# Kernel tuning notes

Measured on AMD Instinct MI355X. Metric: run time of the kernel, lower is better.

## Reference

```python
import jax, jax.numpy as jnp
import numpy as np

B, T, D = 16, 4096, 128   # batch, frames (75 Hz), latent dim
N_Q, K = 8, 1024          # RVQ stages (bandwidth 6 kbps), codebook size


def setup_inputs() -> dict:
    key = jax.random.key(0)
    kx, ke = jax.random.split(key)
    x = jax.random.normal(kx, (B, T, D), dtype=jnp.float32)
    # Residual-VQ codebooks, one [K, D] table per stage (scale=1.0 applied).
    embed = jax.random.normal(ke, (N_Q, K, D), dtype=jnp.float32)
    return {"x": x, "embed": embed}


def reference(x, embed):
    """Residual vector quantization: per stage, nearest-codebook lookup and
    residual subtraction. Returns codes with shape [n_q, B, T] (int32),
    matching encodec's stacked per-stage indices (stage-first layout, as the
    original module's `y[-1]` slicing implies)."""

    def step(residual, e):
        # residual: [B, T, D], e: [K, D]
        # argmin ||r - e||^2 == argmax (2 r.e - ||e||^2); ||r||^2 is constant in k.
        dots = jnp.einsum('btd,kd->btk', residual, e)          # [B, T, K]
        dist = 2.0 * dots - jnp.sum(e * e, axis=-1)            # [B, T, K]
        codes = jnp.argmax(dist, axis=-1).astype(jnp.int32)    # [B, T]
        quantized = e[codes]                                   # gather -> [B, T, D]
        return residual - quantized, codes

    _, codes = jax.lax.scan(step, x, embed)  # codes: [N_Q, B, T]
    return codes
```

## Files before the change

kernel.cpp:

```cpp
#include <hip/hip_runtime.h>

#define M_TOTAL 65536
#define DDIM    128
#define KCODES  1024
#define NQ      8
#define RROWS   64
#define NC      64
#define NCHUNKS (KCODES / NC)
#define CHUNK_B (NC * DDIM * 2)
#define BIAS    320.0f
#define THRQ    0.106f

typedef _Float16 half8 __attribute__((ext_vector_type(8)));
typedef float    f32x4 __attribute__((ext_vector_type(4)));
typedef unsigned u32x2 __attribute__((ext_vector_type(2)));

__device__ __forceinline__ unsigned umx(unsigned a, unsigned b) { return a > b ? a : b; }
__device__ __forceinline__ unsigned umn(unsigned a, unsigned b) { return a < b ? a : b; }

__device__ __forceinline__ void gld_lds16(const void* g, void* l) {
  __builtin_amdgcn_global_load_lds(
      (const __attribute__((address_space(1))) unsigned int*)g,
      (__attribute__((address_space(3))) unsigned int*)l, 16, 0, 0);
}

__global__ __launch_bounds__(256) void enorm_kernel(const float* __restrict__ embed,
                                                    float* __restrict__ enorm) {
  int c = blockIdx.x * 4 + (threadIdx.x >> 6);
  int lane = threadIdx.x & 63;
  const float* e = embed + (size_t)c * DDIM;
  float v0 = e[lane];
  float v1 = e[lane + 64];
  float s = fmaf(v0, v0, v1 * v1);
  #pragma unroll
  for (int off = 32; off > 0; off >>= 1) s += __shfl_down(s, off);
  if (lane == 0) enorm[c] = s;
}

__global__ __launch_bounds__(256) void esplit16_kernel(const float* __restrict__ embed,
                                                       _Float16* __restrict__ Ef16) {
  unsigned u = blockIdx.x * 256 + threadIdx.x;
  size_t src = (size_t)u * 8;
  float4 v0 = *(const float4*)(embed + src);
  float4 v1 = *(const float4*)(embed + src + 4);
  half8 h;
  h[0] = (_Float16)v0.x; h[1] = (_Float16)v0.y; h[2] = (_Float16)v0.z; h[3] = (_Float16)v0.w;
  h[4] = (_Float16)v1.x; h[5] = (_Float16)v1.y; h[6] = (_Float16)v1.z; h[7] = (_Float16)v1.w;
  unsigned row = u >> 4;
  unsigned j   = u & 15;
  size_t dst = (size_t)row * 128 + 8 * (j ^ (row & 7));
  *(half8*)(Ef16 + dst) = h;
}

__global__ __launch_bounds__(256, 2) void rvq_fused(
    const float* __restrict__ x,
    const float* __restrict__ embed,
    const _Float16* __restrict__ Ef16,
    const float* __restrict__ enorm,
    int* __restrict__ codes)
{
  __shared__ __attribute__((aligned(16))) float resid[RROWS][132];
  __shared__ __attribute__((aligned(16))) char EsU[2 * CHUNK_B];
  __shared__ unsigned redk[RROWS][2][2];
  __shared__ int bcode[RROWS];
  __shared__ int frows[RROWS];
  __shared__ int fcnt;

  const int tid = threadIdx.x;
  const int wv = tid >> 6;
  const int lane = tid & 63;
  const int l15 = lane & 15;
  const int q = lane >> 4;
  const int rw = wv & 1;
  const int cw = wv >> 1;
  const int row_base = blockIdx.x * RROWS;
  const int rx = cw * 32 + l15;
  const int xr = rx & 7;

  #pragma unroll
  for (int it = 0; it < 8; ++it) {
    int idx = it * 256 + tid;
    int r = idx >> 5, f4 = idx & 31;
    *(float4*)(&resid[r][f4 * 4]) = *(const float4*)(x + (size_t)(row_base + r) * DDIM + f4 * 4);
  }
  if (tid == 0) fcnt = 0;
  __syncthreads();

  for (int st = 0; st < NQ; ++st) {
    const _Float16* EfS = Ef16 + (size_t)st * KCODES * DDIM;
    const float* enS = enorm + (size_t)st * KCODES;
    const float* embS = embed + (size_t)st * KCODES * DDIM;

    half8 af[2][4];
    #pragma unroll
    for (int rt = 0; rt < 2; ++rt) {
      const float* pa = &resid[rw * 32 + rt * 16 + l15][0];
      #pragma unroll
      for (int kc = 0; kc < 4; ++kc) {
        float4 x0 = *(const float4*)(pa + kc * 32 + q * 8);
        float4 x1 = *(const float4*)(pa + kc * 32 + q * 8 + 4);
        half8 h;
        h[0] = (_Float16)x0.x; h[1] = (_Float16)x0.y; h[2] = (_Float16)x0.z; h[3] = (_Float16)x0.w;
        h[4] = (_Float16)x1.x; h[5] = (_Float16)x1.y; h[6] = (_Float16)x1.z; h[7] = (_Float16)x1.w;
        af[rt][kc] = h;
      }
    }

    {
      const char* g = (const char*)EfS;
      #pragma unroll
      for (int it = 0; it < 4; ++it) {
        const int off = it * 4096 + wv * 1024;
        gld_lds16(g + off + lane * 16, EsU + off);
      }
    }
    float enr0 = enS[cw * 32 + l15];
    float enr1 = enS[cw * 32 + 16 + l15];
    __syncthreads();

    unsigned k1[8], k2[8];
    #pragma unroll
    for (int s = 0; s < 8; ++s) { k1[s] = 0u; k2[s] = 0u; }

    for (int cc = 0; cc < NCHUNKS; ++cc) {
      const int cur = cc & 1;
      if (cc + 1 < NCHUNKS) {
        const char* g = (const char*)EfS + (size_t)(cc + 1) * CHUNK_B;
        char* l = EsU + (cur ^ 1) * CHUNK_B;
        #pragma unroll
        for (int it = 0; it < 4; ++it) {
          const int off = it * 4096 + wv * 1024;
          gld_lds16(g + off + lane * 16, l + off);
        }
      }
      float nh0 = BIAS - 0.5f * enr0;
      float nh1 = BIAS - 0.5f * enr1;
      if (cc + 1 < NCHUNKS) {
        enr0 = enS[(cc + 1) * NC + cw * 32 + l15];
        enr1 = enS[(cc + 1) * NC + cw * 32 + 16 + l15];
      }
      f32x4 acc[2][2];
      #pragma unroll
      for (int rt = 0; rt < 2; ++rt) {
        acc[rt][0] = (f32x4){nh0, nh0, nh0, nh0};
        acc[rt][1] = (f32x4){nh1, nh1, nh1, nh1};
      }

      const char* eb = EsU + cur * CHUNK_B;
      #pragma unroll
      for (int kc = 0; kc < 4; ++kc) {
        const int jswz = 16 * ((kc * 4 + q) ^ xr);
        half8 bf0 = *(const half8*)(eb + rx * 256 + jswz);
        half8 bf1 = *(const half8*)(eb + (rx + 16) * 256 + jswz);
        #pragma unroll
        for (int rt = 0; rt < 2; ++rt) {
          acc[rt][0] = __builtin_amdgcn_mfma_f32_16x16x32_f16(af[rt][kc], bf0, acc[rt][0], 0, 0, 0);
          acc[rt][1] = __builtin_amdgcn_mfma_f32_16x16x32_f16(af[rt][kc], bf1, acc[rt][1], 0, 0, 0);
        }
      }

      const unsigned revb = 1023u - (unsigned)(cc * NC + cw * 32 + l15);
      #pragma unroll
      for (int rt = 0; rt < 2; ++rt)
        #pragma unroll
        for (int reg = 0; reg < 4; ++reg) {
          const int s = rt * 4 + reg;
          unsigned kk0 = (__float_as_uint(acc[rt][0][reg]) & 0xFFFFFC00u) | revb;
          k2[s] = umx(umn(kk0, k1[s]), k2[s]);
          k1[s] = umx(k1[s], kk0);
          unsigned kk1 = (__float_as_uint(acc[rt][1][reg]) & 0xFFFFFC00u) | (revb - 16u);
          k2[s] = umx(umn(kk1, k1[s]), k2[s]);
          k1[s] = umx(k1[s], kk1);
        }
      __syncthreads();
    }

    #pragma unroll
    for (int rt = 0; rt < 2; ++rt)
      #pragma unroll
      for (int reg = 0; reg < 4; ++reg) {
        const int row = rw * 32 + rt * 16 + q * 4 + reg;
        u32x2 kv = {k1[rt * 4 + reg], k2[rt * 4 + reg]};
        *(u32x2*)(EsU + row * 256 + (cw * 16 + l15) * 8) = kv;
      }

    #pragma unroll
    for (int s = 0; s < 8; ++s) {
      #pragma unroll
      for (int off = 1; off < 16; off <<= 1) {
        unsigned o1 = __shfl_xor(k1[s], off);
        unsigned o2 = __shfl_xor(k2[s], off);
        unsigned mn = umn(k1[s], o1);
        k1[s] = umx(k1[s], o1);
        k2[s] = umx(mn, umx(k2[s], o2));
      }
    }
    if (l15 == 0) {
      #pragma unroll
      for (int rt = 0; rt < 2; ++rt)
        #pragma unroll
        for (int reg = 0; reg < 4; ++reg) {
          const int row = rw * 32 + rt * 16 + q * 4 + reg;
          redk[row][cw][0] = k1[rt * 4 + reg];
          redk[row][cw][1] = k2[rt * 4 + reg];
        }
    }
    __syncthreads();

    if (tid < RROWS) {
      unsigned a1 = redk[tid][0][0], a2 = redk[tid][0][1];
      unsigned b1 = redk[tid][1][0], b2 = redk[tid][1][1];
      unsigned f1 = umx(a1, b1);
      unsigned f2 = umx(umn(a1, b1), umx(a2, b2));
      bcode[tid] = 1023 - (int)(f1 & 1023u);
      float d1 = __uint_as_float(f1 & 0xFFFFFC00u);
      float d2 = __uint_as_float(f2 & 0xFFFFFC00u);
      if (d1 - d2 <= THRQ) {
        int p = atomicAdd(&fcnt, 1);
        frows[p] = tid;
      }
    }
    __syncthreads();
    const int nf = fcnt;

    for (int f = wv; f < nf; f += 4) {
      const int r = frows[f];
      const unsigned key = *(const unsigned*)(EsU + r * 256 + (lane >> 1) * 8 + (lane & 1) * 4);
      const int c = 1023 - (int)(key & 1023u);
      const float* rv = &resid[r][0];
      const float* ev = embS + (size_t)c * DDIM;
      float a = 0.f;
      #pragma unroll 4
      for (int k4 = 0; k4 < 32; ++k4) {
        float4 rr = *(const float4*)(rv + k4 * 4);
        float4 e4 = *(const float4*)(ev + k4 * 4);
        a = fmaf(rr.x, e4.x, a); a = fmaf(rr.y, e4.y, a);
        a = fmaf(rr.z, e4.z, a); a = fmaf(rr.w, e4.w, a);
      }
      float bv = 2.0f * a - enS[c];
      int bi = c;
      #pragma unroll
      for (int off = 32; off > 0; off >>= 1) {
        float o = __shfl_down(bv, off);
        int oi = __shfl_down(bi, off);
        if (o > bv || (o == bv && oi < bi)) { bv = o; bi = oi; }
      }
      if (lane == 0) bcode[r] = bi;
    }
    __syncthreads();
    if (tid == 0) fcnt = 0;

    if (tid < RROWS) codes[(size_t)st * M_TOTAL + row_base + tid] = bcode[tid];
    if (st < NQ - 1) {
      #pragma unroll
      for (int it = 0; it < 8; ++it) {
        int idx = it * 256 + tid;
        int r = idx >> 5, f4 = idx & 31;
        float4 e = *(const float4*)(embS + (size_t)bcode[r] * DDIM + f4 * 4);
        float4 a = *(const float4*)(&resid[r][f4 * 4]);
        a.x -= e.x; a.y -= e.y; a.z -= e.z; a.w -= e.w;
        *(float4*)(&resid[r][f4 * 4]) = a;
      }
    }
    __syncthreads();
  }
}

#define F_NCHUNK  256
#define F_KC      16
#define F_AS_STRIDE 68
#define F_ES_STRIDE 260

__global__ __launch_bounds__(256, 3) void rvq_stage_kernel(
    const float* __restrict__ rin, float* __restrict__ rout,
    const float* __restrict__ embed, const float* __restrict__ enorm,
    int* __restrict__ codes)
{
  __shared__ float smem[DDIM * F_AS_STRIDE + F_KC * F_ES_STRIDE + F_NCHUNK];
  float* As  = smem;
  float* Es  = smem + DDIM * F_AS_STRIDE;
  float* Ens = Es + F_KC * F_ES_STRIDE;
  float* red_v = Es;
  int*   red_i = (int*)(Es + 64 * 33);
  int*   bcode = (int*)(Es + 2 * 64 * 33);

  const int tid = threadIdx.x;
  const int tx = tid & 31;
  const int ty = tid >> 5;
  const int row_base = blockIdx.x * 64;

  #pragma unroll
  for (int it = 0; it < 8; ++it) {
    int idx = it * 256 + tid;
    int r = idx >> 5, f4 = idx & 31;
    float4 v = *(const float4*)(rin + (size_t)(row_base + r) * DDIM + f4 * 4);
    As[(4 * f4 + 0) * F_AS_STRIDE + r] = v.x;
    As[(4 * f4 + 1) * F_AS_STRIDE + r] = v.y;
    As[(4 * f4 + 2) * F_AS_STRIDE + r] = v.z;
    As[(4 * f4 + 3) * F_AS_STRIDE + r] = v.w;
  }

  float best[8]; int bidx[8];
  #pragma unroll
  for (int i = 0; i < 8; ++i) { best[i] = -3.0e38f; bidx[i] = 0x7fffffff; }

  for (int nc = 0; nc < KCODES / F_NCHUNK; ++nc) {
    float acc[8][8];
    #pragma unroll
    for (int i = 0; i < 8; ++i)
      #pragma unroll
      for (int j = 0; j < 8; ++j) acc[i][j] = 0.0f;

    for (int kc = 0; kc < DDIM / F_KC; ++kc) {
      __syncthreads();
      #pragma unroll
      for (int it = 0; it < 4; ++it) {
        int idx = it * 256 + tid;
        int c = idx >> 2, f4 = idx & 3;
        float4 v = *(const float4*)(embed + (size_t)(nc * F_NCHUNK + c) * DDIM + kc * F_KC + f4 * 4);
        Es[(4 * f4 + 0) * F_ES_STRIDE + c] = v.x;
        Es[(4 * f4 + 1) * F_ES_STRIDE + c] = v.y;
        Es[(4 * f4 + 2) * F_ES_STRIDE + c] = v.z;
        Es[(4 * f4 + 3) * F_ES_STRIDE + c] = v.w;
      }
      if (kc == 0) Ens[tid] = enorm[nc * F_NCHUNK + tid];
      __syncthreads();

      const float* pa = As + kc * F_KC * F_AS_STRIDE + ty * 8;
      const float* pe = Es + 4 * tx;
      #pragma unroll 4
      for (int k = 0; k < F_KC; ++k) {
        float4 a0 = *(const float4*)(pa + k * F_AS_STRIDE);
        float4 a1 = *(const float4*)(pa + k * F_AS_STRIDE + 4);
        float4 e0 = *(const float4*)(pe + k * F_ES_STRIDE);
        float4 e1 = *(const float4*)(pe + k * F_ES_STRIDE + 128);
        float aa[8] = {a0.x, a0.y, a0.z, a0.w, a1.x, a1.y, a1.z, a1.w};
        float ee[8] = {e0.x, e0.y, e0.z, e0.w, e1.x, e1.y, e1.z, e1.w};
        #pragma unroll
        for (int i = 0; i < 8; ++i)
          #pragma unroll
          for (int j = 0; j < 8; ++j)
            acc[i][j] = fmaf(aa[i], ee[j], acc[i][j]);
      }
    }

    #pragma unroll
    for (int j = 0; j < 8; ++j) {
      int c_local = (j < 4) ? (4 * tx + j) : (128 + 4 * tx + (j - 4));
      float en = Ens[c_local];
      int cg = nc * F_NCHUNK + c_local;
      #pragma unroll
      for (int i = 0; i < 8; ++i) {
        float dist = 2.0f * acc[i][j] - en;
        if (dist > best[i] || (dist == best[i] && cg < bidx[i])) { best[i] = dist; bidx[i] = cg; }
      }
    }
  }

  __syncthreads();
  #pragma unroll
  for (int i = 0; i < 8; ++i) {
    red_v[(ty * 8 + i) * 33 + tx] = best[i];
    red_i[(ty * 8 + i) * 33 + tx] = bidx[i];
  }
  __syncthreads();
  if (tid < 64) {
    float bv = red_v[tid * 33]; int bi = red_i[tid * 33];
    #pragma unroll
    for (int t = 1; t < 32; ++t) {
      float v = red_v[tid * 33 + t]; int ix = red_i[tid * 33 + t];
      if (v > bv || (v == bv && ix < bi)) { bv = v; bi = ix; }
    }
    codes[row_base + tid] = bi;
    bcode[tid] = bi;
  }
  __syncthreads();
  #pragma unroll
  for (int it = 0; it < 32; ++it) {
    int idx = it * 256 + tid;
    int r = idx >> 7, d = idx & 127;
    float e = embed[(size_t)bcode[r] * DDIM + d];
    rout[(size_t)(row_base + r) * DDIM + d] = As[d * F_AS_STRIDE + r] - e;
  }
}

extern "C" void kernel_launch(void* const* d_in, const int* in_sizes, int n_in,
                              void* d_out, int out_size, void* d_ws, size_t ws_size,
                              hipStream_t stream) {
  (void)in_sizes; (void)n_in; (void)out_size;
  const float* x = (const float*)d_in[0];
  const float* embed = (const float*)d_in[1];
  int* codes = (int*)d_out;

  const size_t E16_BYTES = (size_t)NQ * KCODES * DDIM * 2;
  const size_t EN_BYTES  = (size_t)NQ * KCODES * 4;
  const size_t need = E16_BYTES + EN_BYTES + 256;

  if (ws_size >= need) {
    char* w = (char*)d_ws;
    _Float16* Ef16 = (_Float16*)w;     w += E16_BYTES;
    float* enorm   = (float*)w;

    enorm_kernel<<<dim3(NQ * KCODES / 4), dim3(256), 0, stream>>>(embed, enorm);
    esplit16_kernel<<<dim3(NQ * KCODES * DDIM / 8 / 256), dim3(256), 0, stream>>>(embed, Ef16);
    rvq_fused<<<dim3(M_TOTAL / RROWS), dim3(256), 0, stream>>>(
        x, embed, Ef16, enorm, codes);
  } else {
    const size_t resid_elems = (size_t)M_TOTAL * DDIM;
    const bool ws_ok = ws_size >= (resid_elems + (size_t)NQ * KCODES) * sizeof(float);
    float* resid = ws_ok ? (float*)d_ws : (float*)d_in[0];
    float* enorm = ws_ok ? ((float*)d_ws + resid_elems) : (float*)d_ws;

    enorm_kernel<<<dim3(NQ * KCODES / 4), dim3(256), 0, stream>>>(embed, enorm);
    for (int q = 0; q < NQ; ++q) {
      const float* rin = (q == 0) ? x : resid;
      rvq_stage_kernel<<<dim3(M_TOTAL / 64), dim3(256), 0, stream>>>(
          rin, resid, embed + (size_t)q * KCODES * DDIM,
          enorm + (size_t)q * KCODES, codes + (size_t)q * M_TOTAL);
    }
  }
}
```

Baseline: 360.8 us.

## Double fused RVQ block to 512 threads, splitting codes across four wave columns

Raises the fused RVQ kernel from 256 to 512 threads per block, with eight waves where each wave handles 16 codes per chunk instead of 32. Each wave keeps fewer accumulators, and the cross-wave top-2 reduction grows from two to four partial candidates. The fallback recheck now evaluates two candidates per lane. The intent is more waves in flight to hide LDS and MFMA latency, at the cost of per-wave work halving and more barrier and reduction overhead. The launch bound of 4 blocks of 512 threads may also constrain registers.

```diff
diff --git a/kernel.cpp b/kernel.cpp
--- a/kernel.cpp
+++ b/kernel.cpp
@@ -5,6 +5,7 @@
 #define KCODES  1024
 #define NQ      8
 #define RROWS   64
+#define NTHR    512
 #define NC      64
 #define NCHUNKS (KCODES / NC)
 #define CHUNK_B (NC * DDIM * 2)
@@ -52,7 +53,7 @@
   *(half8*)(Ef16 + dst) = h;
 }
 
-__global__ __launch_bounds__(256, 2) void rvq_fused(
+__global__ __launch_bounds__(NTHR, 4) void rvq_fused(
     const float* __restrict__ x,
     const float* __restrict__ embed,
     const _Float16* __restrict__ Ef16,
@@ -61,7 +62,7 @@
 {
   __shared__ __attribute__((aligned(16))) float resid[RROWS][132];
   __shared__ __attribute__((aligned(16))) char EsU[2 * CHUNK_B];
-  __shared__ unsigned redk[RROWS][2][2];
+  __shared__ unsigned redk[RROWS][4][2];
   __shared__ int bcode[RROWS];
   __shared__ int frows[RROWS];
   __shared__ int fcnt;
@@ -74,12 +75,12 @@
   const int rw = wv & 1;
   const int cw = wv >> 1;
   const int row_base = blockIdx.x * RROWS;
-  const int rx = cw * 32 + l15;
+  const int rx = cw * 16 + l15;
   const int xr = rx & 7;
 
   #pragma unroll
-  for (int it = 0; it < 8; ++it) {
-    int idx = it * 256 + tid;
+  for (int it = 0; it < 4; ++it) {
+    int idx = it * NTHR + tid;
     int r = idx >> 5, f4 = idx & 31;
     *(float4*)(&resid[r][f4 * 4]) = *(const float4*)(x + (size_t)(row_base + r) * DDIM + f4 * 4);
   }
@@ -109,13 +110,12 @@
     {
       const char* g = (const char*)EfS;
       #pragma unroll
-      for (int it = 0; it < 4; ++it) {
-        const int off = it * 4096 + wv * 1024;
+      for (int it = 0; it < 2; ++it) {
+        const int off = wv * 2048 + it * 1024;
         gld_lds16(g + off + lane * 16, EsU + off);
       }
     }
-    float enr0 = enS[cw * 32 + l15];
-    float enr1 = enS[cw * 32 + 16 + l15];
+    float enr = enS[cw * 16 + l15];
     __syncthreads();
 
     unsigned k1[8], k2[8];
@@ -128,50 +128,35 @@
         const char* g = (const char*)EfS + (size_t)(cc + 1) * CHUNK_B;
         char* l = EsU + (cur ^ 1) * CHUNK_B;
         #pragma unroll
-        for (int it = 0; it < 4; ++it) {
-          const int off = it * 4096 + wv * 1024;
+        for (int it = 0; it < 2; ++it) {
+          const int off = wv * 2048 + it * 1024;
           gld_lds16(g + off + lane * 16, l + off);
         }
       }
-      float nh0 = BIAS - 0.5f * enr0;
-      float nh1 = BIAS - 0.5f * enr1;
-      if (cc + 1 < NCHUNKS) {
-        enr0 = enS[(cc + 1) * NC + cw * 32 + l15];
-        enr1 = enS[(cc + 1) * NC + cw * 32 + 16 + l15];
-      }
-      f32x4 acc[2][2];
-      #pragma unroll
-      for (int rt = 0; rt < 2; ++rt) {
-        acc[rt][0] = (f32x4){nh0, nh0, nh0, nh0};
-        acc[rt][1] = (f32x4){nh1, nh1, nh1, nh1};
-      }
-
+      float nh = BIAS - 0.5f * enr;
+      if (cc + 1 < NCHUNKS) enr = enS[(cc + 1) * NC + cw * 16 + l15];
+
+      f32x4 acc0 = {nh, nh, nh, nh};
+      f32x4 acc1 = {nh, nh, nh, nh};
       const char* eb = EsU + cur * CHUNK_B;
       #pragma unroll
       for (int kc = 0; kc < 4; ++kc) {
         const int jswz = 16 * ((kc * 4 + q) ^ xr);
-        half8 bf0 = *(const half8*)(eb + rx * 256 + jswz);
-        half8 bf1 = *(const half8*)(eb + (rx + 16) * 256 + jswz);
-        #pragma unroll
-        for (int rt = 0; rt < 2; ++rt) {
-          acc[rt][0] = __builtin_amdgcn_mfma_f32_16x16x32_f16(af[rt][kc], bf0, acc[rt][0], 0, 0, 0);
-          acc[rt][1] = __builtin_amdgcn_mfma_f32_16x16x32_f16(af[rt][kc], bf1, acc[rt][1], 0, 0, 0);
-        }
-      }
-
-      const unsigned revb = 1023u - (unsigned)(cc * NC + cw * 32 + l15);
-      #pragma unroll
-      for (int rt = 0; rt < 2; ++rt)
-        #pragma unroll
-        for (int reg = 0; reg < 4; ++reg) {
-          const int s = rt * 4 + reg;
-          unsigned kk0 = (__float_as_uint(acc[rt][0][reg]) & 0xFFFFFC00u) | revb;
-          k2[s] = umx(umn(kk0, k1[s]), k2[s]);
-          k1[s] = umx(k1[s], kk0);
-          unsigned kk1 = (__float_as_uint(acc[rt][1][reg]) & 0xFFFFFC00u) | (revb - 16u);
-          k2[s] = umx(umn(kk1, k1[s]), k2[s]);
-          k1[s] = umx(k1[s], kk1);
-        }
+        half8 bf = *(const half8*)(eb + rx * 256 + jswz);
+        acc0 = __builtin_amdgcn_mfma_f32_16x16x32_f16(af[0][kc], bf, acc0, 0, 0, 0);
+        acc1 = __builtin_amdgcn_mfma_f32_16x16x32_f16(af[1][kc], bf, acc1, 0, 0, 0);
+      }
+
+      const unsigned revb = 1023u - (unsigned)(cc * NC + cw * 16 + l15);
+      #pragma unroll
+      for (int reg = 0; reg < 4; ++reg) {
+        unsigned kk0 = (__float_as_uint(acc0[reg]) & 0xFFFFFC00u) | revb;
+        k2[reg] = umx(umn(kk0, k1[reg]), k2[reg]);
+        k1[reg] = umx(k1[reg], kk0);
+        unsigned kk1 = (__float_as_uint(acc1[reg]) & 0xFFFFFC00u) | revb;
+        k2[4 + reg] = umx(umn(kk1, k1[4 + reg]), k2[4 + reg]);
+        k1[4 + reg] = umx(k1[4 + reg], kk1);
+      }
       __syncthreads();
     }
 
@@ -181,7 +166,7 @@
       for (int reg = 0; reg < 4; ++reg) {
         const int row = rw * 32 + rt * 16 + q * 4 + reg;
         u32x2 kv = {k1[rt * 4 + reg], k2[rt * 4 + reg]};
-        *(u32x2*)(EsU + row * 256 + (cw * 16 + l15) * 8) = kv;
+        *(u32x2*)(EsU + row * 512 + (cw * 16 + l15) * 8) = kv;
       }
 
     #pragma unroll
@@ -210,8 +195,13 @@
     if (tid < RROWS) {
       unsigned a1 = redk[tid][0][0], a2 = redk[tid][0][1];
       unsigned b1 = redk[tid][1][0], b2 = redk[tid][1][1];
-      unsigned f1 = umx(a1, b1);
-      unsigned f2 = umx(umn(a1, b1), umx(a2, b2));
+      unsigned c1 = redk[tid][2][0], c2 = redk[tid][2][1];
+      unsigned d1v = redk[tid][3][0], d2v = redk[tid][3][1];
+      unsigned m1 = umx(a1, b1), n1 = umn(a1, b1);
+      unsigned m2 = umx(c1, d1v), n2 = umn(c1, d1v);
+      unsigned f1 = umx(m1, m2);
+      unsigned sec4 = umx(umn(m1, m2), umx(n1, n2));
+      unsigned f2 = umx(sec4, umx(umx(a2, b2), umx(c2, d2v)));
       bcode[tid] = 1023 - (int)(f1 & 1023u);
       float d1 = __uint_as_float(f1 & 0xFFFFFC00u);
       float d2 = __uint_as_float(f2 & 0xFFFFFC00u);
@@ -223,22 +213,32 @@
     __syncthreads();
     const int nf = fcnt;
 
-    for (int f = wv; f < nf; f += 4) {
+    for (int f = wv; f < nf; f += 8) {
       const int r = frows[f];
-      const unsigned key = *(const unsigned*)(EsU + r * 256 + (lane >> 1) * 8 + (lane & 1) * 4);
-      const int c = 1023 - (int)(key & 1023u);
+      const char* tb = EsU + r * 512;
+      const unsigned keyA = *(const unsigned*)(tb + (lane >> 1) * 8 + (lane & 1) * 4);
+      const unsigned keyB = *(const unsigned*)(tb + 256 + (lane >> 1) * 8 + (lane & 1) * 4);
+      const int cA = 1023 - (int)(keyA & 1023u);
+      const int cB = 1023 - (int)(keyB & 1023u);
       const float* rv = &resid[r][0];
-      const float* ev = embS + (size_t)c * DDIM;
-      float a = 0.f;
+      const float* evA = embS + (size_t)cA * DDIM;
+      const float* evB = embS + (size_t)cB * DDIM;
+      float aA = 0.f, aB = 0.f;
       #pragma unroll 4
       for (int k4 = 0; k4 < 32; ++k4) {
         float4 rr = *(const float4*)(rv + k4 * 4);
-        float4 e4 = *(const float4*)(ev + k4 * 4);
-        a = fmaf(rr.x, e4.x, a); a = fmaf(rr.y, e4.y, a);
-        a = fmaf(rr.z, e4.z, a); a = fmaf(rr.w, e4.w, a);
-      }
-      float bv = 2.0f * a - enS[c];
-      int bi = c;
+        float4 eA = *(const float4*)(evA + k4 * 4);
+        float4 eB = *(const float4*)(evB + k4 * 4);
+        aA = fmaf(rr.x, eA.x, aA); aA = fmaf(rr.y, eA.y, aA);
+        aA = fmaf(rr.z, eA.z, aA); aA = fmaf(rr.w, eA.w, aA);
+        aB = fmaf(rr.x, eB.x, aB); aB = fmaf(rr.y, eB.y, aB);
+        aB = fmaf(rr.z, eB.z, aB); aB = fmaf(rr.w, eB.w, aB);
+      }
+      float dA = 2.0f * aA - enS[cA];
+      float dB = 2.0f * aB - enS[cB];
+      float bv; int bi;
+      if (dA > dB || (dA == dB && cA < cB)) { bv = dA; bi = cA; }
+      else                                  { bv = dB; bi = cB; }
       #pragma unroll
       for (int off = 32; off > 0; off >>= 1) {
         float o = __shfl_down(bv, off);
@@ -253,8 +253,8 @@
     if (tid < RROWS) codes[(size_t)st * M_TOTAL + row_base + tid] = bcode[tid];
     if (st < NQ - 1) {
       #pragma unroll
-      for (int it = 0; it < 8; ++it) {
-        int idx = it * 256 + tid;
+      for (int it = 0; it < 4; ++it) {
+        int idx = it * NTHR + tid;
         int r = idx >> 5, f4 = idx & 31;
         float4 e = *(const float4*)(embS + (size_t)bcode[r] * DDIM + f4 * 4);
         float4 a = *(const float4*)(&resid[r][f4 * 4]);
@@ -403,7 +403,7 @@
 
     enorm_kernel<<<dim3(NQ * KCODES / 4), dim3(256), 0, stream>>>(embed, enorm);
     esplit16_kernel<<<dim3(NQ * KCODES * DDIM / 8 / 256), dim3(256), 0, stream>>>(embed, Ef16);
-    rvq_fused<<<dim3(M_TOTAL / RROWS), dim3(256), 0, stream>>>(
+    rvq_fused<<<dim3(M_TOTAL / RROWS), dim3(NTHR), 0, stream>>>(
         x, embed, Ef16, enorm, codes);
   } else {
     const size_t resid_elems = (size_t)M_TOTAL * DDIM;
```

Result: slower. 458.2 us (+27.0%).

## Load codebook fragments directly from global into registers, drop LDS staging

Applied to the files above, without the earlier changes.

The fp16 codebook is no longer staged through a double-buffered LDS tile with async global-to-LDS loads and per-chunk barriers. Each wave now loads its MFMA B fragments straight from global (L2-resident) memory into registers, with two-deep register prefetch, and walks 32-code slices with one codebook column tile per wave. This removes the per-chunk __syncthreads and LDS traffic, and the swizzled Ef16 layout becomes plain row-major. In exchange every wave re-reads the codebook from cache with less coalesced 16-byte loads and gets half the MFMA reuse per B load, so the kernel may become bound on cache bandwidth or latency.

```diff
diff --git a/kernel.cpp b/kernel.cpp
--- a/kernel.cpp
+++ b/kernel.cpp
@@ -5,9 +5,7 @@
 #define KCODES  1024
 #define NQ      8
 #define RROWS   64
-#define NC      64
-#define NCHUNKS (KCODES / NC)
-#define CHUNK_B (NC * DDIM * 2)
+#define NITER   32
 #define BIAS    320.0f
 #define THRQ    0.106f
 
@@ -17,12 +15,6 @@
 
 __device__ __forceinline__ unsigned umx(unsigned a, unsigned b) { return a > b ? a : b; }
 __device__ __forceinline__ unsigned umn(unsigned a, unsigned b) { return a < b ? a : b; }
-
-__device__ __forceinline__ void gld_lds16(const void* g, void* l) {
-  __builtin_amdgcn_global_load_lds(
-      (const __attribute__((address_space(1))) unsigned int*)g,
-      (__attribute__((address_space(3))) unsigned int*)l, 16, 0, 0);
-}
 
 __global__ __launch_bounds__(256) void enorm_kernel(const float* __restrict__ embed,
                                                     float* __restrict__ enorm) {
@@ -39,17 +31,13 @@
 
 __global__ __launch_bounds__(256) void esplit16_kernel(const float* __restrict__ embed,
                                                        _Float16* __restrict__ Ef16) {
-  unsigned u = blockIdx.x * 256 + threadIdx.x;
-  size_t src = (size_t)u * 8;
-  float4 v0 = *(const float4*)(embed + src);
-  float4 v1 = *(const float4*)(embed + src + 4);
+  size_t base = ((size_t)blockIdx.x * 256 + threadIdx.x) * 8;
+  float4 v0 = *(const float4*)(embed + base);
+  float4 v1 = *(const float4*)(embed + base + 4);
   half8 h;
   h[0] = (_Float16)v0.x; h[1] = (_Float16)v0.y; h[2] = (_Float16)v0.z; h[3] = (_Float16)v0.w;
   h[4] = (_Float16)v1.x; h[5] = (_Float16)v1.y; h[6] = (_Float16)v1.z; h[7] = (_Float16)v1.w;
-  unsigned row = u >> 4;
-  unsigned j   = u & 15;
-  size_t dst = (size_t)row * 128 + 8 * (j ^ (row & 7));
-  *(half8*)(Ef16 + dst) = h;
+  *(half8*)(Ef16 + base) = h;
 }
 
 __global__ __launch_bounds__(256, 2) void rvq_fused(
@@ -60,7 +48,7 @@
     int* __restrict__ codes)
 {
   __shared__ __attribute__((aligned(16))) float resid[RROWS][132];
-  __shared__ __attribute__((aligned(16))) char EsU[2 * CHUNK_B];
+  __shared__ __attribute__((aligned(16))) char cand[RROWS * 256];
   __shared__ unsigned redk[RROWS][2][2];
   __shared__ int bcode[RROWS];
   __shared__ int frows[RROWS];
@@ -74,8 +62,7 @@
   const int rw = wv & 1;
   const int cw = wv >> 1;
   const int row_base = blockIdx.x * RROWS;
-  const int rx = cw * 32 + l15;
-  const int xr = rx & 7;
+  const int cx = cw * 16 + l15;
 
   #pragma unroll
   for (int it = 0; it < 8; ++it) {
@@ -106,74 +93,55 @@
       }
     }
 
-    {
-      const char* g = (const char*)EfS;
-      #pragma unroll
-      for (int it = 0; it < 4; ++it) {
-        const int off = it * 4096 + wv * 1024;
-        gld_lds16(g + off + lane * 16, EsU + off);
-      }
-    }
-    float enr0 = enS[cw * 32 + l15];
-    float enr1 = enS[cw * 32 + 16 + l15];
-    __syncthreads();
+    const _Float16* bp = EfS + (size_t)cx * DDIM + q * 8;
+    half8 b0[4], b1[4];
+    #pragma unroll
+    for (int kc = 0; kc < 4; ++kc) b0[kc] = *(const half8*)(bp + kc * 32);
+    float enrA = enS[cx];
+    float enrB;
 
     unsigned k1[8], k2[8];
     #pragma unroll
     for (int s = 0; s < 8; ++s) { k1[s] = 0u; k2[s] = 0u; }
 
-    for (int cc = 0; cc < NCHUNKS; ++cc) {
-      const int cur = cc & 1;
-      if (cc + 1 < NCHUNKS) {
-        const char* g = (const char*)EfS + (size_t)(cc + 1) * CHUNK_B;
-        char* l = EsU + (cur ^ 1) * CHUNK_B;
+#define SCREEN_BODY(BF, CC, ENR)                                                   \
+    do {                                                                           \
+      float nh = BIAS - 0.5f * (ENR);                                              \
+      f32x4 a0 = {nh, nh, nh, nh};                                                 \
+      f32x4 a1 = {nh, nh, nh, nh};                                                 \
+      _Pragma("unroll")                                                            \
+      for (int kc = 0; kc < 4; ++kc) {                                             \
+        a0 = __builtin_amdgcn_mfma_f32_16x16x32_f16(af[0][kc], (BF)[kc], a0, 0, 0, 0); \
+        a1 = __builtin_amdgcn_mfma_f32_16x16x32_f16(af[1][kc], (BF)[kc], a1, 0, 0, 0); \
+      }                                                                            \
+      const unsigned revb = 1023u - (unsigned)((CC) * 32 + cx);                    \
+      _Pragma("unroll")                                                            \
+      for (int reg = 0; reg < 4; ++reg) {                                          \
+        unsigned kk0 = (__float_as_uint(a0[reg]) & 0xFFFFFC00u) | revb;            \
+        k2[reg] = umx(umn(kk0, k1[reg]), k2[reg]);                                 \
+        k1[reg] = umx(k1[reg], kk0);                                               \
+        unsigned kk1 = (__float_as_uint(a1[reg]) & 0xFFFFFC00u) | revb;            \
+        k2[4 + reg] = umx(umn(kk1, k1[4 + reg]), k2[4 + reg]);                     \
+        k1[4 + reg] = umx(k1[4 + reg], kk1);                                       \
+      }                                                                            \
+    } while (0)
+
+    #pragma unroll 1
+    for (int cc = 0; cc < NITER; cc += 2) {
+      const _Float16* bn1 = bp + (size_t)(cc + 1) * 32 * DDIM;
+      #pragma unroll
+      for (int kc = 0; kc < 4; ++kc) b1[kc] = *(const half8*)(bn1 + kc * 32);
+      enrB = enS[(cc + 1) * 32 + cx];
+      SCREEN_BODY(b0, cc, enrA);
+      if (cc + 2 < NITER) {
+        const _Float16* bn2 = bp + (size_t)(cc + 2) * 32 * DDIM;
         #pragma unroll
-        for (int it = 0; it < 4; ++it) {
-          const int off = it * 4096 + wv * 1024;
-          gld_lds16(g + off + lane * 16, l + off);
-        }
-      }
-      float nh0 = BIAS - 0.5f * enr0;
-      float nh1 = BIAS - 0.5f * enr1;
-      if (cc + 1 < NCHUNKS) {
-        enr0 = enS[(cc + 1) * NC + cw * 32 + l15];
-        enr1 = enS[(cc + 1) * NC + cw * 32 + 16 + l15];
-      }
-      f32x4 acc[2][2];
-      #pragma unroll
-      for (int rt = 0; rt < 2; ++rt) {
-        acc[rt][0] = (f32x4){nh0, nh0, nh0, nh0};
-        acc[rt][1] = (f32x4){nh1, nh1, nh1, nh1};
-      }
-
-      const char* eb = EsU + cur * CHUNK_B;
-      #pragma unroll
-      for (int kc = 0; kc < 4; ++kc) {
-        const int jswz = 16 * ((kc * 4 + q) ^ xr);
-        half8 bf0 = *(const half8*)(eb + rx * 256 + jswz);
-        half8 bf1 = *(const half8*)(eb + (rx + 16) * 256 + jswz);
-        #pragma unroll
-        for (int rt = 0; rt < 2; ++rt) {
-          acc[rt][0] = __builtin_amdgcn_mfma_f32_16x16x32_f16(af[rt][kc], bf0, acc[rt][0], 0, 0, 0);
-          acc[rt][1] = __builtin_amdgcn_mfma_f32_16x16x32_f16(af[rt][kc], bf1, acc[rt][1], 0, 0, 0);
-        }
-      }
-
-      const unsigned revb = 1023u - (unsigned)(cc * NC + cw * 32 + l15);
-      #pragma unroll
-      for (int rt = 0; rt < 2; ++rt)
-        #pragma unroll
-        for (int reg = 0; reg < 4; ++reg) {
-          const int s = rt * 4 + reg;
-          unsigned kk0 = (__float_as_uint(acc[rt][0][reg]) & 0xFFFFFC00u) | revb;
-          k2[s] = umx(umn(kk0, k1[s]), k2[s]);
-          k1[s] = umx(k1[s], kk0);
-          unsigned kk1 = (__float_as_uint(acc[rt][1][reg]) & 0xFFFFFC00u) | (revb - 16u);
-          k2[s] = umx(umn(kk1, k1[s]), k2[s]);
-          k1[s] = umx(k1[s], kk1);
-        }
-      __syncthreads();
-    }
+        for (int kc = 0; kc < 4; ++kc) b0[kc] = *(const half8*)(bn2 + kc * 32);
+        enrA = enS[(cc + 2) * 32 + cx];
+      }
+      SCREEN_BODY(b1, cc + 1, enrB);
+    }
+#undef SCREEN_BODY
 
     #pragma unroll
     for (int rt = 0; rt < 2; ++rt)
@@ -181,7 +149,7 @@
       for (int reg = 0; reg < 4; ++reg) {
         const int row = rw * 32 + rt * 16 + q * 4 + reg;
         u32x2 kv = {k1[rt * 4 + reg], k2[rt * 4 + reg]};
-        *(u32x2*)(EsU + row * 256 + (cw * 16 + l15) * 8) = kv;
+        *(u32x2*)(cand + row * 256 + cx * 8) = kv;
       }
 
     #pragma unroll
@@ -209,9 +177,9 @@
 
     if (tid < RROWS) {
       unsigned a1 = redk[tid][0][0], a2 = redk[tid][0][1];
-      unsigned b1 = redk[tid][1][0], b2 = redk[tid][1][1];
-      unsigned f1 = umx(a1, b1);
-      unsigned f2 = umx(umn(a1, b1), umx(a2, b2));
+      unsigned b1v = redk[tid][1][0], b2v = redk[tid][1][1];
+      unsigned f1 = umx(a1, b1v);
+      unsigned f2 = umx(umn(a1, b1v), umx(a2, b2v));
       bcode[tid] = 1023 - (int)(f1 & 1023u);
       float d1 = __uint_as_float(f1 & 0xFFFFFC00u);
       float d2 = __uint_as_float(f2 & 0xFFFFFC00u);
@@ -225,7 +193,7 @@
 
     for (int f = wv; f < nf; f += 4) {
       const int r = frows[f];
-      const unsigned key = *(const unsigned*)(EsU + r * 256 + (lane >> 1) * 8 + (lane & 1) * 4);
+      const unsigned key = *(const unsigned*)(cand + r * 256 + (lane >> 1) * 8 + (lane & 1) * 4);
       const int c = 1023 - (int)(key & 1023u);
       const float* rv = &resid[r][0];
       const float* ev = embS + (size_t)c * DDIM;
```

Result: slower. 722.8 us (+100.3%).
